# Kernel tuning notes

Measured on AMD Instinct MI355X. Metric: run time of the kernel, lower is better.

The kernel has to match this reference:

```python
import jax, jax.numpy as jnp
import numpy as np
from jax import lax

N_NODES = 100000
N_EDGES = 1600000
NUM_GRAPHS = 2000
F_IN = 64
HIDDEN = 64
NUM_LAYERS = 3
K = 7
NUM_CLASSES = 10


def setup_inputs() -> dict:
    key = jax.random.key(0)
    ks = jax.random.split(key, 16)
    x = jax.random.normal(ks[0], (N_NODES, F_IN), jnp.float32)
    edge_index = jax.random.randint(ks[1], (2, N_EDGES), 0, N_NODES)
    batch = jnp.sort(jax.random.randint(ks[2], (N_NODES,), 0, NUM_GRAPHS))
    s = 1.0 / np.sqrt(HIDDEN)
    p = lambda k_, sh: jax.random.uniform(k_, sh, jnp.float32, -s, s)
    return dict(
        x=x, edge_index=edge_index, batch=batch,
        W1l=p(ks[3], (F_IN, HIDDEN)), b1=p(ks[4], (HIDDEN,)), W1r=p(ks[5], (F_IN, HIDDEN)),
        W2l=p(ks[6], (HIDDEN, HIDDEN)), b2=p(ks[7], (HIDDEN,)), W2r=p(ks[8], (HIDDEN, HIDDEN)),
        W3l=p(ks[9], (HIDDEN, HIDDEN)), b3=p(ks[10], (HIDDEN,)), W3r=p(ks[11], (HIDDEN, HIDDEN)),
        conv1d_w=p(ks[12], (32, HIDDEN, NUM_LAYERS)), conv1d_b=jnp.zeros((32,), jnp.float32),
        lin1_w=p(ks[13], (32 * (K - NUM_LAYERS + 1), HIDDEN)), lin1_b=jnp.zeros((HIDDEN,), jnp.float32),
        lin2_w=p(ks[14], (HIDDEN, NUM_CLASSES)), lin2_b=jnp.zeros((NUM_CLASSES,), jnp.float32),
    )


def _sage(x, src, dst, Wl, b, Wr):
    # PyG SAGEConv (aggr='mean'): lin_l(mean_j x_j) + lin_r(x_i); lin_l carries the bias.
    n = x.shape[0]
    msum = jax.ops.segment_sum(x[src], dst, num_segments=n)          # [N, D] gather+scatter
    cnt = jax.ops.segment_sum(jnp.ones((src.shape[0],), x.dtype), dst, num_segments=n)
    mean = msum / jnp.maximum(cnt, 1.0)[:, None]
    return mean @ Wl + b + x @ Wr


def _sort_pool(x, batch, num_graphs, k):
    # SortAggregation: per graph, sort nodes descending by last feature channel,
    # keep top-k, zero-pad short graphs, flatten to [B, k*D].
    N, D = x.shape
    perm = jnp.lexsort((-x[:, -1], batch))  # primary: graph id, secondary: desc last channel
    sb = batch[perm]
    counts = jax.ops.segment_sum(jnp.ones((N,), jnp.int32), batch, num_segments=num_graphs)
    starts = jnp.concatenate([jnp.zeros((1,), jnp.int32), jnp.cumsum(counts)[:-1]])
    rank = jnp.arange(N, dtype=jnp.int32) - starts[sb]
    valid = rank < k
    b_idx = jnp.where(valid, sb, num_graphs)  # route overflow nodes to dummy row
    r_idx = jnp.where(valid, rank, 0)
    out = jnp.zeros((num_graphs + 1, k, D), x.dtype).at[b_idx, r_idx].set(x[perm])
    return out[:num_graphs].reshape(num_graphs, k * D)


def reference(x, edge_index, batch, W1l, b1, W1r, W2l, b2, W2r, W3l, b3, W3r,
              conv1d_w, conv1d_b, lin1_w, lin1_b, lin2_w, lin2_b):
    src, dst = edge_index[0], edge_index[1]
    h = jax.nn.relu(_sage(x, src, dst, W1l, b1, W1r))
    h = jax.nn.relu(_sage(h, src, dst, W2l, b2, W2r))
    h = jax.nn.relu(_sage(h, src, dst, W3l, b3, W3r))
    g = _sort_pool(h, batch, NUM_GRAPHS, K)                       # [B, K*H]
    g = g.reshape(NUM_GRAPHS, K, HIDDEN).transpose(0, 2, 1)       # [B, H, K]
    c = lax.conv_general_dilated(g, conv1d_w, (1,), 'VALID',
                                 dimension_numbers=('NCH', 'OIH', 'NCH'))
    c = jax.nn.relu(c + conv1d_b[None, :, None])                  # [B, 32, K-ks+1]
    flat = c.reshape(NUM_GRAPHS, -1)
    h1 = jax.nn.relu(flat @ lin1_w + lin1_b)                      # dropout = identity (eval)
    logits = h1 @ lin2_w + lin2_b
    return jax.nn.log_softmax(logits, axis=-1)
```

## Files before the change

kernel.cpp:

```cpp
#include <hip/hip_runtime.h>
#include <hip/hip_bf16.h>

#define NN 100000
#define NE 1600000
#define NG 2000
#define KTOP 7

#define BNODES 128
#define NBKT 782
#define EPB 8192
#define NL1B 196
#define L2CAP 4096

#define GEMM_BLOCKS 768
#define NTILES 1563
#define SMEM_FLOATS (64 * 68 + 2 * 64 * 64)

#define ACC4(A, V) do { A.x += V.x; A.y += V.y; A.z += V.z; A.w += V.w; } while (0)
#define ACC4P(A, U, W) do { A.x += U.x + W.x; A.y += U.y + W.y; \
                            A.z += U.z + W.z; A.w += U.w + W.w; } while (0)

__device__ __forceinline__ void agg_node(const float* __restrict__ XLp, const int* __restrict__ ce,
        int s, int e, int fo, float4& a0, float4& a1, float4& a2, float4& a3) {
    int a = s;
    for (; a + 2 <= e; a += 2) {
        const float4* p0 = (const float4*)(XLp + ((size_t)ce[a] << 6) + fo);
        const float4* p1 = (const float4*)(XLp + ((size_t)ce[a + 1] << 6) + fo);
        float4 u0 = p0[0], u1 = p0[1], u2 = p0[2], u3 = p0[3];
        float4 w0 = p1[0], w1 = p1[1], w2 = p1[2], w3 = p1[3];
        ACC4P(a0, u0, w0); ACC4P(a1, u1, w1); ACC4P(a2, u2, w2); ACC4P(a3, u3, w3);
    }
    if (a < e) {
        const float4* p0 = (const float4*)(XLp + ((size_t)ce[a] << 6) + fo);
        float4 u0 = p0[0], u1 = p0[1], u2 = p0[2], u3 = p0[3];
        ACC4(a0, u0); ACC4(a1, u1); ACC4(a2, u2); ACC4(a3, u3);
    }
}

#define FMA4C(av, B, acc) do { \
    acc[0] = fmaf(av, B.x, acc[0]); acc[1] = fmaf(av, B.y, acc[1]); \
    acc[2] = fmaf(av, B.z, acc[2]); acc[3] = fmaf(av, B.w, acc[3]); } while (0)

__device__ __forceinline__ void gemm_tile(float* As, float* Bl, float* Br,
        int n0, int ty4, int tx4, float b0, float b1v, float b2v, float b3v,
        float* __restrict__ XL, float* __restrict__ T) {
    float accl[4][4] = {{0.f}}, accr[4][4] = {{0.f}};
    for (int kc = 0; kc < 64; kc += 4) {
        float4 Av[4], L[4], R[4];
        #pragma unroll
        for (int i = 0; i < 4; ++i) Av[i] = *(const float4*)&As[(ty4 + i) * 68 + kc];
        #pragma unroll
        for (int j = 0; j < 4; ++j) {
            L[j] = *(const float4*)&Bl[(kc + j) * 64 + tx4];
            R[j] = *(const float4*)&Br[(kc + j) * 64 + tx4];
        }
        #pragma unroll
        for (int i = 0; i < 4; ++i) {
            FMA4C(Av[i].x, L[0], accl[i]); FMA4C(Av[i].y, L[1], accl[i]);
            FMA4C(Av[i].z, L[2], accl[i]); FMA4C(Av[i].w, L[3], accl[i]);
            FMA4C(Av[i].x, R[0], accr[i]); FMA4C(Av[i].y, R[1], accr[i]);
            FMA4C(Av[i].z, R[2], accr[i]); FMA4C(Av[i].w, R[3], accr[i]);
        }
    }
    #pragma unroll
    for (int i = 0; i < 4; ++i) {
        int g = n0 + ty4 + i;
        if (g < NN) {
            *(float4*)&XL[(size_t)g * 64 + tx4] =
                make_float4(accl[i][0], accl[i][1], accl[i][2], accl[i][3]);
            *(float4*)&T[(size_t)g * 64 + tx4] =
                make_float4(accr[i][0] + b0, accr[i][1] + b1v, accr[i][2] + b2v, accr[i][3] + b3v);
        }
    }
}

__device__ __forceinline__ void stage_weights(float* Bl, float* Br,
        const float* __restrict__ Wl, const float* __restrict__ Wr, int t) {
    #pragma unroll
    for (int q = 0; q < 4; ++q) {
        int idx = t + q * 256;
        ((float4*)Bl)[idx] = ((const float4*)Wl)[idx];
        ((float4*)Br)[idx] = ((const float4*)Wr)[idx];
    }
}

__device__ __forceinline__ void gemm_body(int bid, int nblocks, float* smem,
        const float* __restrict__ X, const float* __restrict__ Wl,
        const float* __restrict__ Wr, const float* __restrict__ bias,
        float* __restrict__ XL, float* __restrict__ T) {
    float* As = smem;
    float* Bl = smem + 64 * 68;
    float* Br = Bl + 64 * 64;
    int t = threadIdx.x;
    stage_weights(Bl, Br, Wl, Wr, t);
    int ty4 = (t >> 4) * 4, tx4 = (t & 15) * 4;
    float b0 = bias[tx4 + 0], b1v = bias[tx4 + 1], b2v = bias[tx4 + 2], b3v = bias[tx4 + 3];
    for (int tile = bid; tile < NTILES; tile += nblocks) {
        int n0 = tile * 64;
        #pragma unroll
        for (int q = 0; q < 4; ++q) {
            int f = t + q * 256;
            int node = f >> 4, seg = f & 15;
            int g = n0 + node;
            float4 v = make_float4(0.f, 0.f, 0.f, 0.f);
            if (g < NN) v = *(const float4*)&X[(size_t)g * 64 + seg * 4];
            *(float4*)&As[node * 68 + seg * 4] = v;
        }
        __syncthreads();
        gemm_tile(As, Bl, Br, n0, ty4, tx4, b0, b1v, b2v, b3v, XL, T);
        __syncthreads();
    }
}

__global__ __launch_bounds__(256) void k_aggemm(const float* __restrict__ XL_in,
        float* __restrict__ T, const int* __restrict__ ptr, const int* __restrict__ ce,
        const float* __restrict__ Wl, const float* __restrict__ Wr,
        const float* __restrict__ bias, float* __restrict__ XL_out) {
    __shared__ float smem[SMEM_FLOATS];
    float* As = smem;
    float* Bl = smem + 64 * 68;
    float* Br = Bl + 64 * 64;
    int t = threadIdx.x;
    stage_weights(Bl, Br, Wl, Wr, t);
    int node_l = t >> 2;
    int fo = (t & 3) * 16;
    int ty4 = (t >> 4) * 4, tx4 = (t & 15) * 4;
    float b0 = bias[tx4 + 0], b1v = bias[tx4 + 1], b2v = bias[tx4 + 2], b3v = bias[tx4 + 3];
    for (int tile = blockIdx.x; tile < NTILES; tile += GEMM_BLOCKS) {
        int n0 = tile * 64;
        int i = n0 + node_l;
        float4 h0 = make_float4(0.f, 0.f, 0.f, 0.f), h1 = h0, h2 = h0, h3 = h0;
        if (i < NN) {
            int s = ptr[i], e = ptr[i + 1];
            agg_node(XL_in, ce, s, e, fo, h0, h1, h2, h3);
            float inv = 1.f / fmaxf((float)(e - s), 1.f);
            const float4* tp = (const float4*)(T + ((size_t)i << 6) + fo);
            float4 t0 = tp[0], t1 = tp[1], t2 = tp[2], t3 = tp[3];
            h0.x = fmaxf(h0.x * inv + t0.x, 0.f); h0.y = fmaxf(h0.y * inv + t0.y, 0.f);
            h0.z = fmaxf(h0.z * inv + t0.z, 0.f); h0.w = fmaxf(h0.w * inv + t0.w, 0.f);
            h1.x = fmaxf(h1.x * inv + t1.x, 0.f); h1.y = fmaxf(h1.y * inv + t1.y, 0.f);
            h1.z = fmaxf(h1.z * inv + t1.z, 0.f); h1.w = fmaxf(h1.w * inv + t1.w, 0.f);
            h2.x = fmaxf(h2.x * inv + t2.x, 0.f); h2.y = fmaxf(h2.y * inv + t2.y, 0.f);
            h2.z = fmaxf(h2.z * inv + t2.z, 0.f); h2.w = fmaxf(h2.w * inv + t2.w, 0.f);
            h3.x = fmaxf(h3.x * inv + t3.x, 0.f); h3.y = fmaxf(h3.y * inv + t3.y, 0.f);
            h3.z = fmaxf(h3.z * inv + t3.z, 0.f); h3.w = fmaxf(h3.w * inv + t3.w, 0.f);
        }
        float* dst = &As[node_l * 68 + fo];
        ((float4*)dst)[0] = h0; ((float4*)dst)[1] = h1;
        ((float4*)dst)[2] = h2; ((float4*)dst)[3] = h3;
        __syncthreads();
        gemm_tile(As, Bl, Br, n0, ty4, tx4, b0, b1v, b2v, b3v, XL_out, T);
        __syncthreads();
    }
}

__global__ __launch_bounds__(256) void k_agg3(const float* __restrict__ XL_in,
        float* __restrict__ T, const int* __restrict__ ptr, const int* __restrict__ ce,
        float* __restrict__ key) {
    int t = threadIdx.x;
    int i = blockIdx.x * 64 + (t >> 2);
    int fo = (t & 3) * 16;
    if (i >= NN) return;
    int s = ptr[i], e = ptr[i + 1];
    float4 h0 = make_float4(0.f, 0.f, 0.f, 0.f), h1 = h0, h2 = h0, h3 = h0;
    agg_node(XL_in, ce, s, e, fo, h0, h1, h2, h3);
    float inv = 1.f / fmaxf((float)(e - s), 1.f);
    float4* tp = (float4*)(T + ((size_t)i << 6) + fo);
    float4 t0 = tp[0], t1 = tp[1], t2 = tp[2], t3 = tp[3];
    h0.x = fmaxf(h0.x * inv + t0.x, 0.f); h0.y = fmaxf(h0.y * inv + t0.y, 0.f);
    h0.z = fmaxf(h0.z * inv + t0.z, 0.f); h0.w = fmaxf(h0.w * inv + t0.w, 0.f);
    h1.x = fmaxf(h1.x * inv + t1.x, 0.f); h1.y = fmaxf(h1.y * inv + t1.y, 0.f);
    h1.z = fmaxf(h1.z * inv + t1.z, 0.f); h1.w = fmaxf(h1.w * inv + t1.w, 0.f);
    h2.x = fmaxf(h2.x * inv + t2.x, 0.f); h2.y = fmaxf(h2.y * inv + t2.y, 0.f);
    h2.z = fmaxf(h2.z * inv + t2.z, 0.f); h2.w = fmaxf(h2.w * inv + t2.w, 0.f);
    h3.x = fmaxf(h3.x * inv + t3.x, 0.f); h3.y = fmaxf(h3.y * inv + t3.y, 0.f);
    h3.z = fmaxf(h3.z * inv + t3.z, 0.f); h3.w = fmaxf(h3.w * inv + t3.w, 0.f);
    tp[0] = h0; tp[1] = h1; tp[2] = h2; tp[3] = h3;
    if ((t & 3) == 3) key[i] = h3.w;
}

__global__ __launch_bounds__(256) void k_front(const float* __restrict__ X,
        const float* __restrict__ Wl, const float* __restrict__ Wr,
        const float* __restrict__ bias, float* __restrict__ XL, float* __restrict__ T,
        const int* __restrict__ edst, int* __restrict__ bh,
        const int* __restrict__ bat, int* __restrict__ gstart) {
    __shared__ float smem[SMEM_FLOATS];
    int bid = blockIdx.x, t = threadIdx.x;
    if (bid < GEMM_BLOCKS) {
        gemm_body(bid, GEMM_BLOCKS, smem, X, Wl, Wr, bias, XL, T);
    } else if (bid < GEMM_BLOCKS + NL1B) {
        int bk = bid - GEMM_BLOCKS;
        int* h = (int*)smem;
        for (int q = t; q < NBKT; q += 256) h[q] = 0;
        __syncthreads();
        int e0 = bk * EPB, e1 = min(e0 + EPB, NE);
        for (int e = e0 + t; e < e1; e += 256) atomicAdd(&h[edst[e] >> 7], 1);
        __syncthreads();
        for (int q = t; q < NBKT; q += 256) bh[bk * NBKT + q] = h[q];
    } else {
        int g = (bid - GEMM_BLOCKS - NL1B) * 256 + t;
        if (g <= NG) {
            int lo = 0, hi = NN;
            while (lo < hi) { int mid = (lo + hi) >> 1; if (bat[mid] < g) lo = mid + 1; else hi = mid; }
            gstart[g] = lo;
        }
    }
}

__global__ void k_colscan(int* __restrict__ bh, int* __restrict__ btot) {
    __shared__ int carry;
    int b = blockIdx.x, t = threadIdx.x;
    if (t == 0) carry = 0;
    __syncthreads();
    for (int base = 0; base < NL1B; base += 64) {
        int idx = base + t;
        int v = (idx < NL1B) ? bh[idx * NBKT + b] : 0;
        int x = v;
        #pragma unroll
        for (int off = 1; off < 64; off <<= 1) {
            int y = __shfl_up(x, off);
            if (t >= off) x += y;
        }
        int c = carry;
        if (idx < NL1B) bh[idx * NBKT + b] = c + x - v;
        __syncthreads();
        if (t == 63) carry = c + x;
        __syncthreads();
    }
    if (t == 0) btot[b] = carry;
}

__global__ void k_btscan(const int* __restrict__ btot, int* __restrict__ bstart) {
    __shared__ int s[1024];
    int t = threadIdx.x;
    int v = (t < NBKT) ? btot[t] : 0;
    s[t] = v; __syncthreads();
    for (int off = 1; off < 1024; off <<= 1) {
        int y = (t >= off) ? s[t - off] : 0;
        __syncthreads();
        s[t] += y;
        __syncthreads();
    }
    if (t < NBKT) bstart[t] = s[t] - v;
    if (t == NBKT - 1) bstart[NBKT] = s[t];
}

__global__ __launch_bounds__(256) void k_bscatter(const int* __restrict__ esrc,
        const int* __restrict__ edst, const int* __restrict__ bh,
        const int* __restrict__ bstart, int* __restrict__ ebuf) {
    __shared__ int cur[NBKT];
    int t = threadIdx.x, bk = blockIdx.x;
    for (int q = t; q < NBKT; q += 256) cur[q] = bstart[q] + bh[bk * NBKT + q];
    __syncthreads();
    int e0 = bk * EPB, e1 = min(e0 + EPB, NE);
    for (int e = e0 + t; e < e1; e += 256) {
        int d = edst[e], s = esrc[e];
        int pos = atomicAdd(&cur[d >> 7], 1);
        ebuf[pos] = s | ((d & 127) << 20);
    }
}

__global__ __launch_bounds__(128) void k_bbuild(const int* __restrict__ ebuf,
        const int* __restrict__ bstart, int* __restrict__ ce, int* __restrict__ ptr) {
    __shared__ int lord[L2CAP];
    __shared__ int cnt[BNODES], sc[BNODES], cursor[BNODES];
    int b = blockIdx.x, t = threadIdx.x;
    int base = bstart[b], nb = bstart[b + 1] - base;
    cnt[t] = 0;
    __syncthreads();
    for (int j = t; j < nb; j += 128) atomicAdd(&cnt[ebuf[base + j] >> 20], 1);
    __syncthreads();
    int v = cnt[t]; sc[t] = v; __syncthreads();
    for (int off = 1; off < 128; off <<= 1) {
        int y = (t >= off) ? sc[t - off] : 0;
        __syncthreads();
        sc[t] += y;
        __syncthreads();
    }
    int segend = sc[t], segstart = sc[t] - v;
    cursor[t] = segstart;
    __syncthreads();
    bool fits = (nb <= L2CAP);
    for (int j = t; j < nb; j += 128) {
        int pv = ebuf[base + j];
        int node = pv >> 20;
        int pos = atomicAdd(&cursor[node], 1);
        if (fits) lord[pos] = pv & 0xFFFFF;
        else ce[base + pos] = pv & 0xFFFFF;
    }
    __syncthreads();
    if (fits) {
        for (int a = segstart + 1; a < segend; ++a) {
            int val = lord[a]; int j = a - 1;
            while (j >= segstart && lord[j] > val) { lord[j + 1] = lord[j]; --j; }
            lord[j + 1] = val;
        }
        __syncthreads();
        for (int j = t; j < nb; j += 128) ce[base + j] = lord[j];
    } else {
        for (int a = segstart + 1; a < segend; ++a) {
            int val = ce[base + a]; int j = a - 1;
            while (j >= segstart && ce[base + j] > val) { ce[base + j + 1] = ce[base + j]; --j; }
            ce[base + j + 1] = val;
        }
    }
    int node = b * BNODES + t;
    if (node <= NN) ptr[node] = base + segstart;
}

__global__ __launch_bounds__(256) void k_tail(const float* __restrict__ key,
        const int* __restrict__ gstart, const float* __restrict__ h3,
        const float* __restrict__ cw, const float* __restrict__ cb,
        const float* __restrict__ l1w, const float* __restrict__ l1b,
        const float* __restrict__ l2w, const float* __restrict__ l2b,
        float* __restrict__ out, int G) {
    __shared__ float sw[32 * 64 * 3];
    __shared__ float s2w[64 * 10];
    __shared__ float sg[4][KTOP][64];
    __shared__ float sflat[4][160];
    __shared__ float sh1[4][64];
    __shared__ float slog[4][10];
    int t = threadIdx.x;
    for (int q = t; q < 32 * 64 * 3; q += 256) sw[q] = cw[q];
    for (int q = t; q < 640; q += 256) s2w[q] = l2w[q];
    int wv = t >> 6, lane = t & 63;
    int b = blockIdx.x * 4 + wv;
    {
        int s = gstart[b], e = gstart[b + 1];
        float pk = 3.4e38f; int pi = -1;
        for (int r = 0; r < KTOP; ++r) {
            float bk = -1.f; int bi = -1;
            for (int i = s + lane; i < e; i += 64) {
                float k = key[i];
                bool elig = (k < pk) || (k == pk && i > pi);
                if (elig && (k > bk || (k == bk && (unsigned)i < (unsigned)bi))) { bk = k; bi = i; }
            }
            #pragma unroll
            for (int off = 1; off < 64; off <<= 1) {
                float ok = __shfl_xor(bk, off);
                int   oi = __shfl_xor(bi, off);
                if (ok > bk || (ok == bk && (unsigned)oi < (unsigned)bi)) { bk = ok; bi = oi; }
            }
            sg[wv][r][lane] = (bi >= 0) ? h3[(size_t)bi * 64 + lane] : 0.f;
            pk = bk; pi = bi;
        }
    }
    __syncthreads();
    for (int idx = lane; idx < 160; idx += 64) {
        int o = idx / 5, p = idx % 5;
        float acc = cb[o];
        #pragma unroll
        for (int dt = 0; dt < 3; ++dt) {
            const float* wrow = &sw[(o * 64) * 3 + dt];
            const float* grow = &sg[wv][p + dt][0];
            for (int i = 0; i < 64; ++i) acc = fmaf(wrow[i * 3], grow[i], acc);
        }
        sflat[wv][idx] = fmaxf(acc, 0.f);
    }
    __syncthreads();
    {
        float acc = l1b[lane];
        for (int k = 0; k < 160; ++k) acc = fmaf(sflat[wv][k], l1w[k * 64 + lane], acc);
        sh1[wv][lane] = fmaxf(acc, 0.f);
    }
    __syncthreads();
    if (lane < 10) {
        float acc = l2b[lane];
        for (int k = 0; k < 64; ++k) acc = fmaf(sh1[wv][k], s2w[k * 10 + lane], acc);
        slog[wv][lane] = acc;
    }
    __syncthreads();
    if (lane < 10) {
        float m = -3.4e38f;
        for (int j = 0; j < 10; ++j) m = fmaxf(m, slog[wv][j]);
        float ssum = 0.f;
        for (int j = 0; j < 10; ++j) ssum += expf(slog[wv][j] - m);
        out[b * 10 + lane] = slog[wv][lane] - m - logf(ssum);
    }
}

extern "C" void kernel_launch(void* const* d_in, const int* in_sizes, int n_in,
                              void* d_out, int out_size, void* d_ws, size_t ws_size,
                              hipStream_t stream) {
    const float* x   = (const float*)d_in[0];
    const int*   ei  = (const int*)d_in[1];
    const int*   bat = (const int*)d_in[2];
    const float* W1l = (const float*)d_in[3], *b1 = (const float*)d_in[4], *W1r = (const float*)d_in[5];
    const float* W2l = (const float*)d_in[6], *b2 = (const float*)d_in[7], *W2r = (const float*)d_in[8];
    const float* W3l = (const float*)d_in[9], *b3 = (const float*)d_in[10], *W3r = (const float*)d_in[11];
    const float* cw  = (const float*)d_in[12], *cb  = (const float*)d_in[13];
    const float* l1w = (const float*)d_in[14], *l1b = (const float*)d_in[15];
    const float* l2w = (const float*)d_in[16], *l2b = (const float*)d_in[17];
    float* out = (float*)d_out;
    const int* esrc = ei;
    const int* edst = ei + NE;

    char* w = (char*)d_ws;
    size_t off = 0;
    auto take = [&](size_t bytes) { void* p = w + off; off = (off + bytes + 255) & ~(size_t)255; return p; };
    int*   bh      = (int*)take((size_t)NL1B * NBKT * 4);
    int*   btot    = (int*)take((size_t)NBKT * 4);
    int*   bstart  = (int*)take((size_t)(NBKT + 1) * 4);
    int*   gstart  = (int*)take((size_t)(NG + 1) * 4);
    int*   ebuf    = (int*)take((size_t)NE * 4);
    int*   csr_ptr = (int*)take((size_t)(NN + 1) * 4);
    int*   csr_e   = (int*)take((size_t)NE * 4);
    float* XLa     = (float*)take((size_t)NN * 64 * 4);
    float* XLb     = (float*)take((size_t)NN * 64 * 4);
    float* T       = (float*)take((size_t)NN * 64 * 4);
    float* key     = (float*)take((size_t)NN * 4);

    k_front<<<GEMM_BLOCKS + NL1B + 8, 256, 0, stream>>>(x, W1l, W1r, b1, XLa, T,
                                                        edst, bh, bat, gstart);
    k_colscan<<<NBKT, 64, 0, stream>>>(bh, btot);
    k_btscan <<<1, 1024, 0, stream>>>(btot, bstart);
    k_bscatter<<<NL1B, 256, 0, stream>>>(esrc, edst, bh, bstart, ebuf);
    k_bbuild <<<NBKT, 128, 0, stream>>>(ebuf, bstart, csr_e, csr_ptr);

    k_aggemm<<<GEMM_BLOCKS, 256, 0, stream>>>(XLa, T, csr_ptr, csr_e, W2l, W2r, b2, XLb);
    k_aggemm<<<GEMM_BLOCKS, 256, 0, stream>>>(XLb, T, csr_ptr, csr_e, W3l, W3r, b3, XLa);
    k_agg3<<<NTILES, 256, 0, stream>>>(XLa, T, csr_ptr, csr_e, key);

    k_tail<<<NG / 4, 256, 0, stream>>>(key, gstart, T, cw, cb, l1w, l1b, l2w, l2b, out, NG);
}
```

Measured before the change: 364.9 us.

## Drop shared-memory weight staging and launch one block per node tile

The GEMM-fused kernels no longer stage the two 64x64 weight matrices in LDS. Each thread reads the weights straight from global memory, relying on cache, which cuts LDS per block from about 49KB to about 17KB and adds a launch-bounds occupancy hint. The persistent grid-stride loop over 768 blocks becomes one block per 64-node tile, so every block runs a single aggregation-plus-GEMM pass. Higher occupancy should hide gather latency better, at the cost of repeated global and L1 weight loads inside the inner GEMM loop.

Result: slower. 414.4 us (+13.6%).

```diff
diff --git a/kernel.cpp b/kernel.cpp
--- a/kernel.cpp
+++ b/kernel.cpp
@@ -12,9 +12,8 @@
 #define NL1B 196
 #define L2CAP 4096
 
-#define GEMM_BLOCKS 768
 #define NTILES 1563
-#define SMEM_FLOATS (64 * 68 + 2 * 64 * 64)
+#define SMEM_FLOATS (64 * 68)
 
 #define ACC4(A, V) do { A.x += V.x; A.y += V.y; A.z += V.z; A.w += V.w; } while (0)
 #define ACC4P(A, U, W) do { A.x += U.x + W.x; A.y += U.y + W.y; \
@@ -41,7 +40,8 @@
     acc[0] = fmaf(av, B.x, acc[0]); acc[1] = fmaf(av, B.y, acc[1]); \
     acc[2] = fmaf(av, B.z, acc[2]); acc[3] = fmaf(av, B.w, acc[3]); } while (0)
 
-__device__ __forceinline__ void gemm_tile(float* As, float* Bl, float* Br,
+__device__ __forceinline__ void gemm_tile(const float* As,
+        const float* __restrict__ Wl, const float* __restrict__ Wr,
         int n0, int ty4, int tx4, float b0, float b1v, float b2v, float b3v,
         float* __restrict__ XL, float* __restrict__ T) {
     float accl[4][4] = {{0.f}}, accr[4][4] = {{0.f}};
@@ -51,8 +51,8 @@
         for (int i = 0; i < 4; ++i) Av[i] = *(const float4*)&As[(ty4 + i) * 68 + kc];
         #pragma unroll
         for (int j = 0; j < 4; ++j) {
-            L[j] = *(const float4*)&Bl[(kc + j) * 64 + tx4];
-            R[j] = *(const float4*)&Br[(kc + j) * 64 + tx4];
+            L[j] = *(const float4*)&Wl[(kc + j) * 64 + tx4];
+            R[j] = *(const float4*)&Wr[(kc + j) * 64 + tx4];
         }
         #pragma unroll
         for (int i = 0; i < 4; ++i) {
@@ -74,84 +74,39 @@
     }
 }
 
-__device__ __forceinline__ void stage_weights(float* Bl, float* Br,
-        const float* __restrict__ Wl, const float* __restrict__ Wr, int t) {
-    #pragma unroll
-    for (int q = 0; q < 4; ++q) {
-        int idx = t + q * 256;
-        ((float4*)Bl)[idx] = ((const float4*)Wl)[idx];
-        ((float4*)Br)[idx] = ((const float4*)Wr)[idx];
-    }
-}
-
-__device__ __forceinline__ void gemm_body(int bid, int nblocks, float* smem,
-        const float* __restrict__ X, const float* __restrict__ Wl,
-        const float* __restrict__ Wr, const float* __restrict__ bias,
-        float* __restrict__ XL, float* __restrict__ T) {
-    float* As = smem;
-    float* Bl = smem + 64 * 68;
-    float* Br = Bl + 64 * 64;
-    int t = threadIdx.x;
-    stage_weights(Bl, Br, Wl, Wr, t);
-    int ty4 = (t >> 4) * 4, tx4 = (t & 15) * 4;
-    float b0 = bias[tx4 + 0], b1v = bias[tx4 + 1], b2v = bias[tx4 + 2], b3v = bias[tx4 + 3];
-    for (int tile = bid; tile < NTILES; tile += nblocks) {
-        int n0 = tile * 64;
-        #pragma unroll
-        for (int q = 0; q < 4; ++q) {
-            int f = t + q * 256;
-            int node = f >> 4, seg = f & 15;
-            int g = n0 + node;
-            float4 v = make_float4(0.f, 0.f, 0.f, 0.f);
-            if (g < NN) v = *(const float4*)&X[(size_t)g * 64 + seg * 4];
-            *(float4*)&As[node * 68 + seg * 4] = v;
-        }
-        __syncthreads();
-        gemm_tile(As, Bl, Br, n0, ty4, tx4, b0, b1v, b2v, b3v, XL, T);
-        __syncthreads();
-    }
-}
-
-__global__ __launch_bounds__(256) void k_aggemm(const float* __restrict__ XL_in,
+__global__ __launch_bounds__(256, 6) void k_aggemm(const float* __restrict__ XL_in,
         float* __restrict__ T, const int* __restrict__ ptr, const int* __restrict__ ce,
         const float* __restrict__ Wl, const float* __restrict__ Wr,
         const float* __restrict__ bias, float* __restrict__ XL_out) {
-    __shared__ float smem[SMEM_FLOATS];
-    float* As = smem;
-    float* Bl = smem + 64 * 68;
-    float* Br = Bl + 64 * 64;
+    __shared__ float As[SMEM_FLOATS];
     int t = threadIdx.x;
-    stage_weights(Bl, Br, Wl, Wr, t);
     int node_l = t >> 2;
     int fo = (t & 3) * 16;
+    int n0 = blockIdx.x * 64;
+    int i = n0 + node_l;
+    float4 h0 = make_float4(0.f, 0.f, 0.f, 0.f), h1 = h0, h2 = h0, h3 = h0;
+    if (i < NN) {
+        int s = ptr[i], e = ptr[i + 1];
+        agg_node(XL_in, ce, s, e, fo, h0, h1, h2, h3);
+        float inv = 1.f / fmaxf((float)(e - s), 1.f);
+        const float4* tp = (const float4*)(T + ((size_t)i << 6) + fo);
+        float4 t0 = tp[0], t1 = tp[1], t2 = tp[2], t3 = tp[3];
+        h0.x = fmaxf(h0.x * inv + t0.x, 0.f); h0.y = fmaxf(h0.y * inv + t0.y, 0.f);
+        h0.z = fmaxf(h0.z * inv + t0.z, 0.f); h0.w = fmaxf(h0.w * inv + t0.w, 0.f);
+        h1.x = fmaxf(h1.x * inv + t1.x, 0.f); h1.y = fmaxf(h1.y * inv + t1.y, 0.f);
+        h1.z = fmaxf(h1.z * inv + t1.z, 0.f); h1.w = fmaxf(h1.w * inv + t1.w, 0.f);
+        h2.x = fmaxf(h2.x * inv + t2.x, 0.f); h2.y = fmaxf(h2.y * inv + t2.y, 0.f);
+        h2.z = fmaxf(h2.z * inv + t2.z, 0.f); h2.w = fmaxf(h2.w * inv + t2.w, 0.f);
+        h3.x = fmaxf(h3.x * inv + t3.x, 0.f); h3.y = fmaxf(h3.y * inv + t3.y, 0.f);
+        h3.z = fmaxf(h3.z * inv + t3.z, 0.f); h3.w = fmaxf(h3.w * inv + t3.w, 0.f);
+    }
+    float* dst = &As[node_l * 68 + fo];
+    ((float4*)dst)[0] = h0; ((float4*)dst)[1] = h1;
+    ((float4*)dst)[2] = h2; ((float4*)dst)[3] = h3;
+    __syncthreads();
     int ty4 = (t >> 4) * 4, tx4 = (t & 15) * 4;
     float b0 = bias[tx4 + 0], b1v = bias[tx4 + 1], b2v = bias[tx4 + 2], b3v = bias[tx4 + 3];
-    for (int tile = blockIdx.x; tile < NTILES; tile += GEMM_BLOCKS) {
-        int n0 = tile * 64;
-        int i = n0 + node_l;
-        float4 h0 = make_float4(0.f, 0.f, 0.f, 0.f), h1 = h0, h2 = h0, h3 = h0;
-        if (i < NN) {
-            int s = ptr[i], e = ptr[i + 1];
-            agg_node(XL_in, ce, s, e, fo, h0, h1, h2, h3);
-            float inv = 1.f / fmaxf((float)(e - s), 1.f);
-            const float4* tp = (const float4*)(T + ((size_t)i << 6) + fo);
-            float4 t0 = tp[0], t1 = tp[1], t2 = tp[2], t3 = tp[3];
-            h0.x = fmaxf(h0.x * inv + t0.x, 0.f); h0.y = fmaxf(h0.y * inv + t0.y, 0.f);
-            h0.z = fmaxf(h0.z * inv + t0.z, 0.f); h0.w = fmaxf(h0.w * inv + t0.w, 0.f);
-            h1.x = fmaxf(h1.x * inv + t1.x, 0.f); h1.y = fmaxf(h1.y * inv + t1.y, 0.f);
-            h1.z = fmaxf(h1.z * inv + t1.z, 0.f); h1.w = fmaxf(h1.w * inv + t1.w, 0.f);
-            h2.x = fmaxf(h2.x * inv + t2.x, 0.f); h2.y = fmaxf(h2.y * inv + t2.y, 0.f);
-            h2.z = fmaxf(h2.z * inv + t2.z, 0.f); h2.w = fmaxf(h2.w * inv + t2.w, 0.f);
-            h3.x = fmaxf(h3.x * inv + t3.x, 0.f); h3.y = fmaxf(h3.y * inv + t3.y, 0.f);
-            h3.z = fmaxf(h3.z * inv + t3.z, 0.f); h3.w = fmaxf(h3.w * inv + t3.w, 0.f);
-        }
-        float* dst = &As[node_l * 68 + fo];
-        ((float4*)dst)[0] = h0; ((float4*)dst)[1] = h1;
-        ((float4*)dst)[2] = h2; ((float4*)dst)[3] = h3;
-        __syncthreads();
-        gemm_tile(As, Bl, Br, n0, ty4, tx4, b0, b1v, b2v, b3v, XL_out, T);
-        __syncthreads();
-    }
+    gemm_tile(As, Wl, Wr, n0, ty4, tx4, b0, b1v, b2v, b3v, XL_out, T);
 }
 
 __global__ __launch_bounds__(256) void k_agg3(const float* __restrict__ XL_in,
@@ -179,18 +134,31 @@
     if ((t & 3) == 3) key[i] = h3.w;
 }
 
-__global__ __launch_bounds__(256) void k_front(const float* __restrict__ X,
+__global__ __launch_bounds__(256, 6) void k_front(const float* __restrict__ X,
         const float* __restrict__ Wl, const float* __restrict__ Wr,
         const float* __restrict__ bias, float* __restrict__ XL, float* __restrict__ T,
         const int* __restrict__ edst, int* __restrict__ bh,
         const int* __restrict__ bat, int* __restrict__ gstart) {
-    __shared__ float smem[SMEM_FLOATS];
+    __shared__ float As[SMEM_FLOATS];
     int bid = blockIdx.x, t = threadIdx.x;
-    if (bid < GEMM_BLOCKS) {
-        gemm_body(bid, GEMM_BLOCKS, smem, X, Wl, Wr, bias, XL, T);
-    } else if (bid < GEMM_BLOCKS + NL1B) {
-        int bk = bid - GEMM_BLOCKS;
-        int* h = (int*)smem;
+    if (bid < NTILES) {
+        int n0 = bid * 64;
+        #pragma unroll
+        for (int q = 0; q < 4; ++q) {
+            int f = t + q * 256;
+            int node = f >> 4, seg = f & 15;
+            int g = n0 + node;
+            float4 v = make_float4(0.f, 0.f, 0.f, 0.f);
+            if (g < NN) v = *(const float4*)&X[(size_t)g * 64 + seg * 4];
+            *(float4*)&As[node * 68 + seg * 4] = v;
+        }
+        __syncthreads();
+        int ty4 = (t >> 4) * 4, tx4 = (t & 15) * 4;
+        float b0 = bias[tx4 + 0], b1v = bias[tx4 + 1], b2v = bias[tx4 + 2], b3v = bias[tx4 + 3];
+        gemm_tile(As, Wl, Wr, n0, ty4, tx4, b0, b1v, b2v, b3v, XL, T);
+    } else if (bid < NTILES + NL1B) {
+        int bk = bid - NTILES;
+        int* h = (int*)As;
         for (int q = t; q < NBKT; q += 256) h[q] = 0;
         __syncthreads();
         int e0 = bk * EPB, e1 = min(e0 + EPB, NE);
@@ -198,7 +166,7 @@
         __syncthreads();
         for (int q = t; q < NBKT; q += 256) bh[bk * NBKT + q] = h[q];
     } else {
-        int g = (bid - GEMM_BLOCKS - NL1B) * 256 + t;
+        int g = (bid - NTILES - NL1B) * 256 + t;
         if (g <= NG) {
             int lo = 0, hi = NN;
             while (lo < hi) { int mid = (lo + hi) >> 1; if (bat[mid] < g) lo = mid + 1; else hi = mid; }
@@ -410,15 +378,15 @@
     float* T       = (float*)take((size_t)NN * 64 * 4);
     float* key     = (float*)take((size_t)NN * 4);
 
-    k_front<<<GEMM_BLOCKS + NL1B + 8, 256, 0, stream>>>(x, W1l, W1r, b1, XLa, T,
-                                                        edst, bh, bat, gstart);
+    k_front<<<NTILES + NL1B + 8, 256, 0, stream>>>(x, W1l, W1r, b1, XLa, T,
+                                                   edst, bh, bat, gstart);
     k_colscan<<<NBKT, 64, 0, stream>>>(bh, btot);
     k_btscan <<<1, 1024, 0, stream>>>(btot, bstart);
     k_bscatter<<<NL1B, 256, 0, stream>>>(esrc, edst, bh, bstart, ebuf);
     k_bbuild <<<NBKT, 128, 0, stream>>>(ebuf, bstart, csr_e, csr_ptr);
 
-    k_aggemm<<<GEMM_BLOCKS, 256, 0, stream>>>(XLa, T, csr_ptr, csr_e, W2l, W2r, b2, XLb);
-    k_aggemm<<<GEMM_BLOCKS, 256, 0, stream>>>(XLb, T, csr_ptr, csr_e, W3l, W3r, b3, XLa);
+    k_aggemm<<<NTILES, 256, 0, stream>>>(XLa, T, csr_ptr, csr_e, W2l, W2r, b2, XLb);
+    k_aggemm<<<NTILES, 256, 0, stream>>>(XLb, T, csr_ptr, csr_e, W3l, W3r, b3, XLa);
     k_agg3<<<NTILES, 256, 0, stream>>>(XLa, T, csr_ptr, csr_e, key);
 
     k_tail<<<NG / 4, 256, 0, stream>>>(key, gstart, T, cw, cb, l1w, l1b, l2w, l2b, out, NG);
```

## Compute layer-3 aggregation only for top-k nodes using scalar sort key

Applied to the files above, without the earlier changes.

The full 64-wide layer-3 mean aggregation over all nodes is replaced with a scalar pass over only the last channel, which yields the sort key. The layer-2 GEMM epilogue now also writes that channel's pre-aggregation value and residual term. Top-k selection moves to its own kernel, and the full 64-feature aggregation runs only for the 14000 selected nodes before the dense head. This removes most of the gather traffic of the last layer, at the cost of three extra small launches and a second traversal of the edge index list.

Measured after the change: 330.1 us. 1.11x faster.

```diff
diff --git a/kernel.cpp b/kernel.cpp
--- a/kernel.cpp
+++ b/kernel.cpp
@@ -37,13 +37,27 @@
     }
 }
 
+__device__ __forceinline__ void relu_mean_res(float inv, const float4* tp,
+        float4& h0, float4& h1, float4& h2, float4& h3) {
+    float4 t0 = tp[0], t1 = tp[1], t2 = tp[2], t3 = tp[3];
+    h0.x = fmaxf(h0.x * inv + t0.x, 0.f); h0.y = fmaxf(h0.y * inv + t0.y, 0.f);
+    h0.z = fmaxf(h0.z * inv + t0.z, 0.f); h0.w = fmaxf(h0.w * inv + t0.w, 0.f);
+    h1.x = fmaxf(h1.x * inv + t1.x, 0.f); h1.y = fmaxf(h1.y * inv + t1.y, 0.f);
+    h1.z = fmaxf(h1.z * inv + t1.z, 0.f); h1.w = fmaxf(h1.w * inv + t1.w, 0.f);
+    h2.x = fmaxf(h2.x * inv + t2.x, 0.f); h2.y = fmaxf(h2.y * inv + t2.y, 0.f);
+    h2.z = fmaxf(h2.z * inv + t2.z, 0.f); h2.w = fmaxf(h2.w * inv + t2.w, 0.f);
+    h3.x = fmaxf(h3.x * inv + t3.x, 0.f); h3.y = fmaxf(h3.y * inv + t3.y, 0.f);
+    h3.z = fmaxf(h3.z * inv + t3.z, 0.f); h3.w = fmaxf(h3.w * inv + t3.w, 0.f);
+}
+
 #define FMA4C(av, B, acc) do { \
     acc[0] = fmaf(av, B.x, acc[0]); acc[1] = fmaf(av, B.y, acc[1]); \
     acc[2] = fmaf(av, B.z, acc[2]); acc[3] = fmaf(av, B.w, acc[3]); } while (0)
 
-__device__ __forceinline__ void gemm_tile(float* As, float* Bl, float* Br,
+__device__ __forceinline__ void gemm_tile(const float* As, const float* Bl, const float* Br,
         int n0, int ty4, int tx4, float b0, float b1v, float b2v, float b3v,
-        float* __restrict__ XL, float* __restrict__ T) {
+        float* __restrict__ XL, float* __restrict__ T,
+        float* __restrict__ kc_out, float* __restrict__ tc_out) {
     float accl[4][4] = {{0.f}}, accr[4][4] = {{0.f}};
     for (int kc = 0; kc < 64; kc += 4) {
         float4 Av[4], L[4], R[4];
@@ -70,6 +84,10 @@
                 make_float4(accl[i][0], accl[i][1], accl[i][2], accl[i][3]);
             *(float4*)&T[(size_t)g * 64 + tx4] =
                 make_float4(accr[i][0] + b0, accr[i][1] + b1v, accr[i][2] + b2v, accr[i][3] + b3v);
+            if (kc_out && tx4 == 60) {
+                kc_out[g] = accl[i][3];
+                tc_out[g] = accr[i][3] + b3v;
+            }
         }
     }
 }
@@ -107,7 +125,7 @@
             *(float4*)&As[node * 68 + seg * 4] = v;
         }
         __syncthreads();
-        gemm_tile(As, Bl, Br, n0, ty4, tx4, b0, b1v, b2v, b3v, XL, T);
+        gemm_tile(As, Bl, Br, n0, ty4, tx4, b0, b1v, b2v, b3v, XL, T, nullptr, nullptr);
         __syncthreads();
     }
 }
@@ -115,7 +133,8 @@
 __global__ __launch_bounds__(256) void k_aggemm(const float* __restrict__ XL_in,
         float* __restrict__ T, const int* __restrict__ ptr, const int* __restrict__ ce,
         const float* __restrict__ Wl, const float* __restrict__ Wr,
-        const float* __restrict__ bias, float* __restrict__ XL_out) {
+        const float* __restrict__ bias, float* __restrict__ XL_out,
+        float* __restrict__ kc_out, float* __restrict__ tc_out) {
     __shared__ float smem[SMEM_FLOATS];
     float* As = smem;
     float* Bl = smem + 64 * 68;
@@ -134,49 +153,73 @@
             int s = ptr[i], e = ptr[i + 1];
             agg_node(XL_in, ce, s, e, fo, h0, h1, h2, h3);
             float inv = 1.f / fmaxf((float)(e - s), 1.f);
-            const float4* tp = (const float4*)(T + ((size_t)i << 6) + fo);
-            float4 t0 = tp[0], t1 = tp[1], t2 = tp[2], t3 = tp[3];
-            h0.x = fmaxf(h0.x * inv + t0.x, 0.f); h0.y = fmaxf(h0.y * inv + t0.y, 0.f);
-            h0.z = fmaxf(h0.z * inv + t0.z, 0.f); h0.w = fmaxf(h0.w * inv + t0.w, 0.f);
-            h1.x = fmaxf(h1.x * inv + t1.x, 0.f); h1.y = fmaxf(h1.y * inv + t1.y, 0.f);
-            h1.z = fmaxf(h1.z * inv + t1.z, 0.f); h1.w = fmaxf(h1.w * inv + t1.w, 0.f);
-            h2.x = fmaxf(h2.x * inv + t2.x, 0.f); h2.y = fmaxf(h2.y * inv + t2.y, 0.f);
-            h2.z = fmaxf(h2.z * inv + t2.z, 0.f); h2.w = fmaxf(h2.w * inv + t2.w, 0.f);
-            h3.x = fmaxf(h3.x * inv + t3.x, 0.f); h3.y = fmaxf(h3.y * inv + t3.y, 0.f);
-            h3.z = fmaxf(h3.z * inv + t3.z, 0.f); h3.w = fmaxf(h3.w * inv + t3.w, 0.f);
+            relu_mean_res(inv, (const float4*)(T + ((size_t)i << 6) + fo), h0, h1, h2, h3);
         }
         float* dst = &As[node_l * 68 + fo];
         ((float4*)dst)[0] = h0; ((float4*)dst)[1] = h1;
         ((float4*)dst)[2] = h2; ((float4*)dst)[3] = h3;
         __syncthreads();
-        gemm_tile(As, Bl, Br, n0, ty4, tx4, b0, b1v, b2v, b3v, XL_out, T);
-        __syncthreads();
-    }
-}
-
-__global__ __launch_bounds__(256) void k_agg3(const float* __restrict__ XL_in,
-        float* __restrict__ T, const int* __restrict__ ptr, const int* __restrict__ ce,
-        float* __restrict__ key) {
-    int t = threadIdx.x;
-    int i = blockIdx.x * 64 + (t >> 2);
-    int fo = (t & 3) * 16;
+        gemm_tile(As, Bl, Br, n0, ty4, tx4, b0, b1v, b2v, b3v, XL_out, T, kc_out, tc_out);
+        __syncthreads();
+    }
+}
+
+__global__ __launch_bounds__(256) void k_key(const float* __restrict__ keycol,
+        const float* __restrict__ tcol, const int* __restrict__ ptr,
+        const int* __restrict__ ce, float* __restrict__ key) {
+    int i = blockIdx.x * 256 + threadIdx.x;
     if (i >= NN) return;
     int s = ptr[i], e = ptr[i + 1];
+    float acc = 0.f;
+    int a = s;
+    for (; a + 2 <= e; a += 2) acc += keycol[ce[a]] + keycol[ce[a + 1]];
+    if (a < e) acc += keycol[ce[a]];
+    float inv = 1.f / fmaxf((float)(e - s), 1.f);
+    key[i] = fmaxf(acc * inv + tcol[i], 0.f);
+}
+
+__global__ __launch_bounds__(256) void k_topk(const float* __restrict__ key,
+        const int* __restrict__ gstart, int* __restrict__ idx7, int G) {
+    int wv = threadIdx.x >> 6, lane = threadIdx.x & 63;
+    int b = blockIdx.x * 4 + wv;
+    if (b >= G) return;
+    int s = gstart[b], e = gstart[b + 1];
+    float pk = 3.4e38f; int pi = -1;
+    for (int r = 0; r < KTOP; ++r) {
+        float bk = -1.f; int bi = -1;
+        for (int i = s + lane; i < e; i += 64) {
+            float k = key[i];
+            bool elig = (k < pk) || (k == pk && i > pi);
+            if (elig && (k > bk || (k == bk && (unsigned)i < (unsigned)bi))) { bk = k; bi = i; }
+        }
+        #pragma unroll
+        for (int off = 1; off < 64; off <<= 1) {
+            float ok = __shfl_xor(bk, off);
+            int   oi = __shfl_xor(bi, off);
+            if (ok > bk || (ok == bk && (unsigned)oi < (unsigned)bi)) { bk = ok; bi = oi; }
+        }
+        if (lane == 0) idx7[b * KTOP + r] = bi;
+        pk = bk; pi = bi;
+    }
+}
+
+__global__ __launch_bounds__(256) void k_aggW(const float* __restrict__ XL_in,
+        const float* __restrict__ T, const int* __restrict__ ptr, const int* __restrict__ ce,
+        const int* __restrict__ idx7, float* __restrict__ H3W) {
+    int t = threadIdx.x;
+    int j = blockIdx.x * 64 + (t >> 2);
+    int fo = (t & 3) * 16;
+    if (j >= NG * KTOP) return;
+    int i = idx7[j];
     float4 h0 = make_float4(0.f, 0.f, 0.f, 0.f), h1 = h0, h2 = h0, h3 = h0;
-    agg_node(XL_in, ce, s, e, fo, h0, h1, h2, h3);
-    float inv = 1.f / fmaxf((float)(e - s), 1.f);
-    float4* tp = (float4*)(T + ((size_t)i << 6) + fo);
-    float4 t0 = tp[0], t1 = tp[1], t2 = tp[2], t3 = tp[3];
-    h0.x = fmaxf(h0.x * inv + t0.x, 0.f); h0.y = fmaxf(h0.y * inv + t0.y, 0.f);
-    h0.z = fmaxf(h0.z * inv + t0.z, 0.f); h0.w = fmaxf(h0.w * inv + t0.w, 0.f);
-    h1.x = fmaxf(h1.x * inv + t1.x, 0.f); h1.y = fmaxf(h1.y * inv + t1.y, 0.f);
-    h1.z = fmaxf(h1.z * inv + t1.z, 0.f); h1.w = fmaxf(h1.w * inv + t1.w, 0.f);
-    h2.x = fmaxf(h2.x * inv + t2.x, 0.f); h2.y = fmaxf(h2.y * inv + t2.y, 0.f);
-    h2.z = fmaxf(h2.z * inv + t2.z, 0.f); h2.w = fmaxf(h2.w * inv + t2.w, 0.f);
-    h3.x = fmaxf(h3.x * inv + t3.x, 0.f); h3.y = fmaxf(h3.y * inv + t3.y, 0.f);
-    h3.z = fmaxf(h3.z * inv + t3.z, 0.f); h3.w = fmaxf(h3.w * inv + t3.w, 0.f);
-    tp[0] = h0; tp[1] = h1; tp[2] = h2; tp[3] = h3;
-    if ((t & 3) == 3) key[i] = h3.w;
+    if (i >= 0) {
+        int s = ptr[i], e = ptr[i + 1];
+        agg_node(XL_in, ce, s, e, fo, h0, h1, h2, h3);
+        float inv = 1.f / fmaxf((float)(e - s), 1.f);
+        relu_mean_res(inv, (const float4*)(T + ((size_t)i << 6) + fo), h0, h1, h2, h3);
+    }
+    float4* dst = (float4*)(H3W + (size_t)j * 64 + fo);
+    dst[0] = h0; dst[1] = h1; dst[2] = h2; dst[3] = h3;
 }
 
 __global__ __launch_bounds__(256) void k_front(const float* __restrict__ X,
@@ -308,8 +351,7 @@
     if (node <= NN) ptr[node] = base + segstart;
 }
 
-__global__ __launch_bounds__(256) void k_tail(const float* __restrict__ key,
-        const int* __restrict__ gstart, const float* __restrict__ h3,
+__global__ __launch_bounds__(256) void k_head(const float* __restrict__ H3W,
         const float* __restrict__ cw, const float* __restrict__ cb,
         const float* __restrict__ l1w, const float* __restrict__ l1b,
         const float* __restrict__ l2w, const float* __restrict__ l2b,
@@ -325,26 +367,8 @@
     for (int q = t; q < 640; q += 256) s2w[q] = l2w[q];
     int wv = t >> 6, lane = t & 63;
     int b = blockIdx.x * 4 + wv;
-    {
-        int s = gstart[b], e = gstart[b + 1];
-        float pk = 3.4e38f; int pi = -1;
-        for (int r = 0; r < KTOP; ++r) {
-            float bk = -1.f; int bi = -1;
-            for (int i = s + lane; i < e; i += 64) {
-                float k = key[i];
-                bool elig = (k < pk) || (k == pk && i > pi);
-                if (elig && (k > bk || (k == bk && (unsigned)i < (unsigned)bi))) { bk = k; bi = i; }
-            }
-            #pragma unroll
-            for (int off = 1; off < 64; off <<= 1) {
-                float ok = __shfl_xor(bk, off);
-                int   oi = __shfl_xor(bi, off);
-                if (ok > bk || (ok == bk && (unsigned)oi < (unsigned)bi)) { bk = ok; bi = oi; }
-            }
-            sg[wv][r][lane] = (bi >= 0) ? h3[(size_t)bi * 64 + lane] : 0.f;
-            pk = bk; pi = bi;
-        }
-    }
+    for (int r = 0; r < KTOP; ++r)
+        sg[wv][r][lane] = H3W[(size_t)(b * KTOP + r) * 64 + lane];
     __syncthreads();
     for (int idx = lane; idx < 160; idx += 64) {
         int o = idx / 5, p = idx % 5;
@@ -402,13 +426,17 @@
     int*   btot    = (int*)take((size_t)NBKT * 4);
     int*   bstart  = (int*)take((size_t)(NBKT + 1) * 4);
     int*   gstart  = (int*)take((size_t)(NG + 1) * 4);
+    int*   idx7    = (int*)take((size_t)NG * KTOP * 4);
     int*   ebuf    = (int*)take((size_t)NE * 4);
     int*   csr_ptr = (int*)take((size_t)(NN + 1) * 4);
     int*   csr_e   = (int*)take((size_t)NE * 4);
     float* XLa     = (float*)take((size_t)NN * 64 * 4);
     float* XLb     = (float*)take((size_t)NN * 64 * 4);
     float* T       = (float*)take((size_t)NN * 64 * 4);
+    float* keycol  = (float*)take((size_t)NN * 4);
+    float* tcol    = (float*)take((size_t)NN * 4);
     float* key     = (float*)take((size_t)NN * 4);
+    float* H3W     = (float*)take((size_t)NG * KTOP * 64 * 4);
 
     k_front<<<GEMM_BLOCKS + NL1B + 8, 256, 0, stream>>>(x, W1l, W1r, b1, XLa, T,
                                                         edst, bh, bat, gstart);
@@ -417,9 +445,13 @@
     k_bscatter<<<NL1B, 256, 0, stream>>>(esrc, edst, bh, bstart, ebuf);
     k_bbuild <<<NBKT, 128, 0, stream>>>(ebuf, bstart, csr_e, csr_ptr);
 
-    k_aggemm<<<GEMM_BLOCKS, 256, 0, stream>>>(XLa, T, csr_ptr, csr_e, W2l, W2r, b2, XLb);
-    k_aggemm<<<GEMM_BLOCKS, 256, 0, stream>>>(XLb, T, csr_ptr, csr_e, W3l, W3r, b3, XLa);
-    k_agg3<<<NTILES, 256, 0, stream>>>(XLa, T, csr_ptr, csr_e, key);
-
-    k_tail<<<NG / 4, 256, 0, stream>>>(key, gstart, T, cw, cb, l1w, l1b, l2w, l2b, out, NG);
-}
+    k_aggemm<<<GEMM_BLOCKS, 256, 0, stream>>>(XLa, T, csr_ptr, csr_e, W2l, W2r, b2, XLb,
+                                              nullptr, nullptr);
+    k_aggemm<<<GEMM_BLOCKS, 256, 0, stream>>>(XLb, T, csr_ptr, csr_e, W3l, W3r, b3, XLa,
+                                              keycol, tcol);
+
+    k_key <<<(NN + 255) / 256, 256, 0, stream>>>(keycol, tcol, csr_ptr, csr_e, key);
+    k_topk<<<(NG + 3) / 4, 256, 0, stream>>>(key, gstart, idx7, NG);
+    k_aggW<<<(NG * KTOP + 63) / 64, 256, 0, stream>>>(XLa, T, csr_ptr, csr_e, idx7, H3W);
+    k_head<<<NG / 4, 256, 0, stream>>>(H3W, cw, cb, l1w, l1b, l2w, l2b, out, NG);
+}
```
